# Performance work log

Measured on AMD Instinct MI355X. Metric: run time of the kernel, lower is better.

## Reference

```python
import jax, jax.numpy as jnp
import numpy as np

FREQ_DIM = 64
BLOCK_DIM = 64
N = 256          # lattice sites
CH = 6           # channel_num -> block diagonals at offsets -1, 0, +1
S = 2 * 16 + CH - 2   # seq_num = 36
BS = 4           # block_size (kron of two 2x2 matrices)
HID = 128
EPS = 1e-5
B = 32

_e = np.eye(2)
_sx = np.array([[0., 1.], [1., 0.]])
_siy = np.array([[0., 1.], [-1., 0.]])
_sz = np.array([[1., 0.], [0., -1.]])
_p = [_e, _sx, _siy, _sz]
KRONS = jnp.asarray(np.stack([np.kron(_p[a], _p[b]) for a in range(4) for b in range(4)]).astype(np.float32))  # (16,4,4)
Z1 = KRONS[12]  # kron(sigma_z, I) used for interaction blocks ('z1')


def _bn(h, g, b):
    # BatchNorm1d in training mode: biased batch statistics over axis 0
    mu = h.mean(axis=0)
    v = h.var(axis=0)
    return g * (h - mu) / jnp.sqrt(v + EPS) + b


def _mlp(x, Win, bin_, Wmid, bmid, Wout, bout, gamma, beta):
    # depth-4 MLP: Lin+ReLU, then (BN,Lin,ReLU) x2, then BN,Lin,ReLU
    h = jax.nn.relu(x @ Win + bin_)
    for i in range(Wmid.shape[0]):
        h = jax.nn.relu(_bn(h, gamma[i], beta[i]) @ Wmid[i] + bmid[i])
    return jax.nn.relu(_bn(h, gamma[-1], beta[-1]) @ Wout + bout)


def _lstm(xs, h0, c0, Wih, Whh, bih, bhh):
    # xs: (B, T, S); torch gate order i, f, g, o
    def step(carry, x_t):
        h, c = carry
        gates = x_t @ Wih.T + h @ Whh.T + (bih + bhh)
        i, f, g, o = jnp.split(gates, 4, axis=-1)
        c = jax.nn.sigmoid(f) * c + jax.nn.sigmoid(i) * jnp.tanh(g)
        h = jax.nn.sigmoid(o) * jnp.tanh(c)
        return (h, c), h
    _, hs = jax.lax.scan(step, (h0, c0), jnp.swapaxes(xs, 0, 1))
    return jnp.swapaxes(hs, 0, 1)


def setup_inputs() -> dict:
    key = jax.random.key(0)
    ks = iter(jax.random.split(key, 48))
    def w(shape, s=0.05):
        return jax.random.normal(next(ks), shape, dtype=jnp.float32) * s
    d = {
        'x': w((B, FREQ_DIM + BLOCK_DIM), 1.0),
        'fd_Win': w((FREQ_DIM, HID)), 'fd_bin': w((HID,)),
        'fd_Wmid': w((2, HID, HID)), 'fd_bmid': w((2, HID)),
        'fd_Wout': w((HID, S)), 'fd_bout': w((S,)),
        'fd_gamma': jnp.ones((3, HID), jnp.float32), 'fd_beta': jnp.zeros((3, HID), jnp.float32),
        'bd_Win': w((BLOCK_DIM, HID)), 'bd_bin': w((HID,)),
        'bd_Wmid': w((2, HID, HID)), 'bd_bmid': w((2, HID)),
        'bd_Wout': w((HID, S)), 'bd_bout': w((S,)),
        'bd_gamma': jnp.ones((3, HID), jnp.float32), 'bd_beta': jnp.zeros((3, HID), jnp.float32),
        'sc_Win': w((S, 1, HID)), 'sc_bin': w((S, HID)),
        'sc_Wmid': w((S, 2, HID, HID)), 'sc_bmid': w((S, 2, HID)),
        'sc_Wout': w((S, HID, N)), 'sc_bout': w((S, N)),
        'sc_gamma': jnp.ones((S, 3, HID), jnp.float32), 'sc_beta': jnp.zeros((S, 3, HID), jnp.float32),
        'lstm_Wih': w((4 * S, S)), 'lstm_Whh': w((4 * S, S)),
        'lstm_bih': w((4 * S,)), 'lstm_bhh': w((4 * S,)),
        'mix_W': w((S, 2 * S)), 'mix_b': w((S,)),
    }
    return d


def reference(x, fd_Win, fd_bin, fd_Wmid, fd_bmid, fd_Wout, fd_bout, fd_gamma, fd_beta,
              bd_Win, bd_bin, bd_Wmid, bd_bmid, bd_Wout, bd_bout, bd_gamma, bd_beta,
              sc_Win, sc_bin, sc_Wmid, sc_bmid, sc_Wout, sc_bout, sc_gamma, sc_beta,
              lstm_Wih, lstm_Whh, lstm_bih, lstm_bhh, mix_W, mix_b):
    Bsz = x.shape[0]
    block = _mlp(x[:, FREQ_DIM:], bd_Win, bd_bin, bd_Wmid, bd_bmid, bd_Wout, bd_bout, bd_gamma, bd_beta)  # (B,S)
    freq = _mlp(x[:, :FREQ_DIM], fd_Win, fd_bin, fd_Wmid, fd_bmid, fd_Wout, fd_bout, fd_gamma, fd_beta)   # (B,S)
    # S independent scalar->N MLPs, batched with vmap over the stacked params
    sc = jax.vmap(_mlp)(freq.T[:, :, None], sc_Win, sc_bin, sc_Wmid, sc_bmid,
                        sc_Wout, sc_bout, sc_gamma, sc_beta)  # (S,B,N)
    freq_seq = jnp.cos(sc).transpose(1, 2, 0)   # (B,N,S)
    seq = _lstm(freq_seq, block, jnp.zeros_like(block), lstm_Wih, lstm_Whh, lstm_bih, lstm_bhh)  # (B,N,S)
    block_seq = jnp.concatenate([jnp.broadcast_to(block[:, :, None], (Bsz, S, N)),
                                 jnp.swapaxes(seq, 1, 2)], axis=1)  # (B,2S,N)
    # 1x1 Conv2d == channel mixing matmul
    mixed = jnp.einsum('bcn,oc->bon', block_seq, mix_W) + mix_b[None, :, None]  # (B,S,N)
    inter = mixed[:, :CH - 2]                          # (B,CH-2,N)
    onsite = mixed[:, CH - 2:].reshape(Bsz, 2, 16, N)  # (B,2,16,N)
    H_int = jnp.einsum('bcn,ij->bcnij', inter, Z1)         # (B,CH-2,N,4,4)
    H_os = jnp.einsum('bgkn,kij->bgnij', onsite, KRONS)    # (B,2,N,4,4) summed over 16 pairs
    half = (CH - 2) // 2
    strips = jnp.concatenate([H_int[:, :half], H_os, H_int[:, half:]], axis=1)  # (B,CH,N,4,4)
    strips = strips.reshape(Bsz, CH // 2, 2, N, BS, BS)
    # banded block assembly: strip i lives on block-diagonal offset i - (CH//2)//2
    grid = jnp.zeros((Bsz, 2, N, N, BS, BS), dtype=x.dtype)
    for i in range(CH // 2):
        o = i - (CH // 2) // 2
        rows = jnp.arange(N - abs(o)) + max(0, -o)
        cols = rows + o
        grid = grid.at[:, :, rows, cols].set(strips[:, i][:, :, rows])
    matrix = grid.transpose(0, 1, 2, 4, 3, 5).reshape(Bsz, 2, N * BS, N * BS)
    return matrix
```

## Files before the change

kernel.cpp:

```cpp
#include <hip/hip_runtime.h>
#include <math.h>

#define EPSF 1e-5f

__device__ __forceinline__ float tanhf_fast(float x) {
    return 1.f - 2.f / (__expf(2.f * x) + 1.f);
}

__device__ void mlp64_body(const float* __restrict__ xin,
                           const float* __restrict__ Win,
                           const float* __restrict__ bin_,
                           const float* __restrict__ Wmid,
                           const float* __restrict__ bmid,
                           const float* __restrict__ Wout,
                           const float* __restrict__ bout,
                           const float* __restrict__ gamma,
                           const float* __restrict__ beta,
                           float* __restrict__ out)
{
    __shared__ float sX[32 * 64];
    __shared__ float sA[32 * 128];
    __shared__ float sB[32 * 128];
    __shared__ float sMu[128], sRs[128];
    int tid = threadIdx.x;

    for (int idx = tid; idx < 32 * 64; idx += 256) {
        int b = idx >> 6, c = idx & 63;
        sX[idx] = xin[b * 128 + c];
    }
    __syncthreads();

    for (int idx = tid; idx < 32 * 128; idx += 256) {
        int b = idx >> 7, j = idx & 127;
        float acc = bin_[j];
        for (int c = 0; c < 64; ++c) acc = fmaf(sX[b * 64 + c], Win[c * 128 + j], acc);
        sA[idx] = fmaxf(acc, 0.f);
    }
    __syncthreads();

    float* cur = sA;
    float* nxt = sB;
    for (int l = 0; l < 3; ++l) {
        if (tid < 128) {
            float s = 0.f, s2 = 0.f;
            for (int b = 0; b < 32; ++b) {
                float v = cur[b * 128 + tid];
                s += v; s2 += v * v;
            }
            float mu = s * (1.f / 32.f);
            float var = s2 * (1.f / 32.f) - mu * mu;
            sMu[tid] = mu;
            sRs[tid] = rsqrtf(var + EPSF);
        }
        __syncthreads();
        for (int idx = tid; idx < 32 * 128; idx += 256) {
            int j = idx & 127;
            cur[idx] = gamma[l * 128 + j] * (cur[idx] - sMu[j]) * sRs[j] + beta[l * 128 + j];
        }
        __syncthreads();
        if (l < 2) {
            for (int idx = tid; idx < 32 * 128; idx += 256) {
                int b = idx >> 7, j = idx & 127;
                float acc = bmid[l * 128 + j];
                for (int c = 0; c < 128; ++c)
                    acc = fmaf(cur[b * 128 + c], Wmid[(l * 128 + c) * 128 + j], acc);
                nxt[idx] = fmaxf(acc, 0.f);
            }
            __syncthreads();
            float* t = cur; cur = nxt; nxt = t;
        } else {
            for (int idx = tid; idx < 32 * 36; idx += 256) {
                int b = idx / 36, j = idx - b * 36;
                float acc = bout[j];
                for (int c = 0; c < 128; ++c)
                    acc = fmaf(cur[b * 128 + c], Wout[c * 36 + j], acc);
                out[idx] = fmaxf(acc, 0.f);
            }
        }
    }
}

__global__ __launch_bounds__(256) void k_mlp2(
    const float* __restrict__ x,
    const float* fdWin, const float* fdbin, const float* fdWmid, const float* fdbmid,
    const float* fdWout, const float* fdbout, const float* fdg, const float* fdbt,
    const float* bdWin, const float* bdbin, const float* bdWmid, const float* bdbmid,
    const float* bdWout, const float* bdbout, const float* bdg, const float* bdbt,
    float* freq, float* blk)
{
    if (blockIdx.x == 0)
        mlp64_body(x + 64, bdWin, bdbin, bdWmid, bdbmid, bdWout, bdbout, bdg, bdbt, blk);
    else
        mlp64_body(x, fdWin, fdbin, fdWmid, fdbmid, fdWout, fdbout, fdg, fdbt, freq);
}

__global__ __launch_bounds__(512) void k_sc(
    const float* __restrict__ freq,
    const float* __restrict__ Win,
    const float* __restrict__ bin_,
    const float* __restrict__ Wmid,
    const float* __restrict__ bmid,
    const float* __restrict__ Wout,
    const float* __restrict__ bout,
    const float* __restrict__ gamma,
    const float* __restrict__ beta,
    float* __restrict__ fseq)
{
    int s = blockIdx.x, tid = threadIdx.x;
    __shared__ float sA[32 * 128];
    __shared__ float sB[32 * 128];
    __shared__ float sMu[128], sRs[128];
    const float* Wm = Wmid + (size_t)s * 2 * 128 * 128;
    const float* Wo = Wout + (size_t)s * 128 * 256;
    const float* gm = gamma + s * 3 * 128;
    const float* bt = beta + s * 3 * 128;

    for (int idx = tid; idx < 32 * 128; idx += 512) {
        int b = idx >> 7, j = idx & 127;
        float acc = fmaf(freq[b * 36 + s], Win[s * 128 + j], bin_[s * 128 + j]);
        sA[idx] = fmaxf(acc, 0.f);
    }
    __syncthreads();

    float* cur = sA;
    float* nxt = sB;
    for (int l = 0; l < 3; ++l) {
        if (tid < 128) {
            float sm = 0.f, s2 = 0.f;
            for (int b = 0; b < 32; ++b) {
                float v = cur[b * 128 + tid];
                sm += v; s2 += v * v;
            }
            float mu = sm * (1.f / 32.f);
            float var = s2 * (1.f / 32.f) - mu * mu;
            sMu[tid] = mu;
            sRs[tid] = rsqrtf(var + EPSF);
        }
        __syncthreads();
        for (int idx = tid; idx < 32 * 128; idx += 512) {
            int j = idx & 127;
            cur[idx] = gm[l * 128 + j] * (cur[idx] - sMu[j]) * sRs[j] + bt[l * 128 + j];
        }
        __syncthreads();
        if (l < 2) {
            for (int idx = tid; idx < 32 * 128; idx += 512) {
                int b = idx >> 7, j = idx & 127;
                float acc = bmid[(s * 2 + l) * 128 + j];
                for (int c = 0; c < 128; ++c)
                    acc = fmaf(cur[b * 128 + c], Wm[(l * 128 + c) * 128 + j], acc);
                nxt[idx] = fmaxf(acc, 0.f);
            }
            __syncthreads();
            float* t = cur; cur = nxt; nxt = t;
        } else {
            for (int idx = tid; idx < 32 * 256; idx += 512) {
                int b = idx >> 8, n = idx & 255;
                float acc = bout[s * 256 + n];
                for (int c = 0; c < 128; ++c)
                    acc = fmaf(cur[b * 128 + c], Wo[c * 256 + n], acc);
                float v = fmaxf(acc, 0.f);
                fseq[((size_t)n * 32 + b) * 36 + s] = cosf(v);
            }
        }
    }
}

__global__ __launch_bounds__(512) void k_xg(
    const float* __restrict__ fseq, const float* __restrict__ Wih,
    const float* __restrict__ bih, const float* __restrict__ bhh,
    float* __restrict__ Xg)
{
    int t = blockIdx.x, tid = threadIdx.x;
    __shared__ float sF[32 * 36];
    for (int idx = tid; idx < 1152; idx += 512) sF[idx] = fseq[(size_t)t * 1152 + idx];
    __syncthreads();
    for (int idx = tid; idx < 32 * 144; idx += 512) {
        int b = idx / 144, j = idx - b * 144;
        float acc = bih[j] + bhh[j];
        #pragma unroll
        for (int s2 = 0; s2 < 36; ++s2)
            acc = fmaf(sF[b * 36 + s2], Wih[j * 36 + s2], acc);
        Xg[((size_t)t * 32 + b) * 144 + j] = acc;
    }
}

__global__ __launch_bounds__(192) void k_lstm(
    const float* __restrict__ Xg, const float* __restrict__ blockIn,
    const float* __restrict__ Whh, float* __restrict__ hseq)
{
    int b = blockIdx.x, tid = threadIdx.x;
    __shared__ float sh[36];
    __shared__ float sg[144];
    float w[36];
    if (tid < 144) {
        #pragma unroll
        for (int k = 0; k < 36; ++k) w[k] = Whh[tid * 36 + k];
    }
    if (tid < 36) sh[tid] = blockIn[b * 36 + tid];
    float c = 0.f;
    float xg = (tid < 144) ? Xg[(size_t)b * 144 + tid] : 0.f;
    const int type = tid / 36;
    __syncthreads();

    for (int t = 0; t < 256; ++t) {
        float act = 0.f;
        if (tid < 144) {
            float a0 = 0.f, a1 = 0.f, a2 = 0.f, a3 = 0.f;
            #pragma unroll
            for (int k = 0; k < 36; k += 4) {
                a0 = fmaf(w[k + 0], sh[k + 0], a0);
                a1 = fmaf(w[k + 1], sh[k + 1], a1);
                a2 = fmaf(w[k + 2], sh[k + 2], a2);
                a3 = fmaf(w[k + 3], sh[k + 3], a3);
            }
            float gate = xg + (a0 + a1) + (a2 + a3);
            float sarg = (type == 2) ? 2.f * gate : gate;
            float sv = 1.f / (1.f + __expf(-sarg));
            act = (type == 2) ? 2.f * sv - 1.f : sv;
        }
        if (t < 255 && tid < 144) xg = Xg[((size_t)(t + 1) * 32 + b) * 144 + tid];
        if (tid < 144) sg[tid] = act;
        __syncthreads();
        if (tid < 36) {
            float iv = sg[tid], fv = sg[36 + tid], gv = sg[72 + tid], ov = sg[108 + tid];
            c = fmaf(fv, c, iv * gv);
            float h = ov * tanhf_fast(c);
            sh[tid] = h;
            hseq[((size_t)b * 256 + t) * 36 + tid] = h;
        }
        __syncthreads();
    }
}

__global__ __launch_bounds__(256) void k_mixed(
    const float* __restrict__ blockIn, const float* __restrict__ hseq,
    const float* __restrict__ mixW, const float* __restrict__ mixb,
    float* __restrict__ mixed)
{
    int wg = blockIdx.x;
    int b = wg / 36, o = wg - b * 36;
    int n = threadIdx.x;
    float acc = mixb[o];
    const float* wrow = mixW + o * 72;
    const float* blk = blockIn + b * 36;
    #pragma unroll
    for (int c = 0; c < 36; ++c) acc = fmaf(wrow[c], blk[c], acc);
    const float* hp = hseq + ((size_t)b * 256 + n) * 36;
    #pragma unroll
    for (int u = 0; u < 36; ++u) acc = fmaf(wrow[36 + u], hp[u], acc);
    mixed[(size_t)wg * 256 + n] = acc;
}

__device__ __forceinline__ float pauliv(int p, int r, int c) {
    switch (p) {
        case 0: return (r == c) ? 1.f : 0.f;
        case 1: return (r != c) ? 1.f : 0.f;
        case 2: return (r == 0 && c == 1) ? 1.f : ((r == 1 && c == 0) ? -1.f : 0.f);
        default: return (r == c) ? ((r == 0) ? 1.f : -1.f) : 0.f;
    }
}

__global__ __launch_bounds__(256) void k_asm(
    const float* __restrict__ mixed, float* __restrict__ out)
{
    int wg = blockIdx.x;
    int n = wg & 255, bg = wg >> 8;
    int g = bg & 1, b = bg >> 1;
    int tid = threadIdx.x;
    __shared__ float sD[16];
    __shared__ float sEdge[2];
    if (tid < 16) {
        int r = tid >> 2, c = tid & 3;
        float acc = 0.f;
        #pragma unroll
        for (int k = 0; k < 16; ++k) {
            float kv = pauliv(k >> 2, r >> 1, c >> 1) * pauliv(k & 3, r & 1, c & 1);
            acc = fmaf(mixed[((size_t)b * 36 + 4 + 16 * g + k) * 256 + n], kv, acc);
        }
        sD[tid] = acc;
    } else if (tid == 16) {
        sEdge[0] = mixed[((size_t)b * 36 + g) * 256 + n];
    } else if (tid == 17) {
        sEdge[1] = mixed[((size_t)b * 36 + 2 + g) * 256 + n];
    }
    __syncthreads();

    float4* outp = (float4*)out + ((size_t)bg * 1024 + 4 * n) * 256;
    int m = tid;
    if (m == n) {
        #pragma unroll
        for (int r = 0; r < 4; ++r)
            outp[r * 256 + m] = make_float4(sD[r * 4 + 0], sD[r * 4 + 1], sD[r * 4 + 2], sD[r * 4 + 3]);
    } else if (m == n - 1) {
        float v = sEdge[0];
        outp[0 * 256 + m] = make_float4(v, 0.f, 0.f, 0.f);
        outp[1 * 256 + m] = make_float4(0.f, v, 0.f, 0.f);
        outp[2 * 256 + m] = make_float4(0.f, 0.f, -v, 0.f);
        outp[3 * 256 + m] = make_float4(0.f, 0.f, 0.f, -v);
    } else if (m == n + 1) {
        float v = sEdge[1];
        outp[0 * 256 + m] = make_float4(v, 0.f, 0.f, 0.f);
        outp[1 * 256 + m] = make_float4(0.f, v, 0.f, 0.f);
        outp[2 * 256 + m] = make_float4(0.f, 0.f, -v, 0.f);
        outp[3 * 256 + m] = make_float4(0.f, 0.f, 0.f, -v);
    } else {
        float4 z = make_float4(0.f, 0.f, 0.f, 0.f);
        #pragma unroll
        for (int r = 0; r < 4; ++r) outp[r * 256 + m] = z;
    }
}

extern "C" void kernel_launch(void* const* d_in, const int* in_sizes, int n_in,
                              void* d_out, int out_size, void* d_ws, size_t ws_size,
                              hipStream_t stream) {
    const float* x      = (const float*)d_in[0];
    const float* fdWin  = (const float*)d_in[1];
    const float* fdbin  = (const float*)d_in[2];
    const float* fdWmid = (const float*)d_in[3];
    const float* fdbmid = (const float*)d_in[4];
    const float* fdWout = (const float*)d_in[5];
    const float* fdbout = (const float*)d_in[6];
    const float* fdg    = (const float*)d_in[7];
    const float* fdbt   = (const float*)d_in[8];
    const float* bdWin  = (const float*)d_in[9];
    const float* bdbin  = (const float*)d_in[10];
    const float* bdWmid = (const float*)d_in[11];
    const float* bdbmid = (const float*)d_in[12];
    const float* bdWout = (const float*)d_in[13];
    const float* bdbout = (const float*)d_in[14];
    const float* bdg    = (const float*)d_in[15];
    const float* bdbt   = (const float*)d_in[16];
    const float* scWin  = (const float*)d_in[17];
    const float* scbin  = (const float*)d_in[18];
    const float* scWmid = (const float*)d_in[19];
    const float* scbmid = (const float*)d_in[20];
    const float* scWout = (const float*)d_in[21];
    const float* scbout = (const float*)d_in[22];
    const float* scg    = (const float*)d_in[23];
    const float* scbt   = (const float*)d_in[24];
    const float* Wih    = (const float*)d_in[25];
    const float* Whh    = (const float*)d_in[26];
    const float* bih    = (const float*)d_in[27];
    const float* bhh    = (const float*)d_in[28];
    const float* mixW   = (const float*)d_in[29];
    const float* mixb   = (const float*)d_in[30];

    float* ws    = (float*)d_ws;
    float* freq  = ws;
    float* blk   = ws + 1152;
    float* fseq  = ws + 2304;
    float* Xg    = ws + 297216;
    float* hseq  = ws + 1476864;
    float* mixed = ws + 1771776;

    k_mlp2<<<2, 256, 0, stream>>>(x,
        fdWin, fdbin, fdWmid, fdbmid, fdWout, fdbout, fdg, fdbt,
        bdWin, bdbin, bdWmid, bdbmid, bdWout, bdbout, bdg, bdbt,
        freq, blk);
    k_sc<<<36, 512, 0, stream>>>(freq, scWin, scbin, scWmid, scbmid,
                                 scWout, scbout, scg, scbt, fseq);
    k_xg<<<256, 512, 0, stream>>>(fseq, Wih, bih, bhh, Xg);
    k_lstm<<<32, 192, 0, stream>>>(Xg, blk, Whh, hseq);
    k_mixed<<<1152, 256, 0, stream>>>(blk, hseq, mixW, mixb, mixed);
    k_asm<<<16384, 256, 0, stream>>>(mixed, (float*)d_out);
}
```

Measured before the change: 375.6 us.

## Fuse all stages into one cooperative persistent kernel with grid syncs

Replaces the six separate launches (MLPs, per-sequence MLPs, input-gate projection, LSTM, channel mixing, banded assembly) with a single cooperative kernel of 256 blocks of 512 threads, using grid.sync between stages. It also overlaps the block MLP with the sequence MLPs, stages a transposed Wih in shared memory, and switches cosf to __cosf. The goal is to remove launch overhead and inter-kernel gaps. The cost is that the 16M-element output assembly now runs on only 256 blocks looping 32 times, and grid syncs leave most blocks idle during the serial LSTM.

```diff
diff --git a/kernel.cpp b/kernel.cpp
--- a/kernel.cpp
+++ b/kernel.cpp
@@ -1,10 +1,30 @@
 #include <hip/hip_runtime.h>
+#include <hip/hip_cooperative_groups.h>
 #include <math.h>
 
+namespace cg = cooperative_groups;
+
 #define EPSF 1e-5f
 
-__device__ __forceinline__ float tanhf_fast(float x) {
-    return 1.f - 2.f / (__expf(2.f * x) + 1.f);
+struct Params {
+    const float *x;
+    const float *fdWin, *fdbin, *fdWmid, *fdbmid, *fdWout, *fdbout, *fdg, *fdbt;
+    const float *bdWin, *bdbin, *bdWmid, *bdbmid, *bdWout, *bdbout, *bdg, *bdbt;
+    const float *scWin, *scbin, *scWmid, *scbmid, *scWout, *scbout, *scg, *scbt;
+    const float *Wih, *Whh, *bih, *bhh, *mixW, *mixb;
+    float *freq, *blk, *fseq, *Xg, *hseq, *mixed, *out;
+};
+
+__device__ __forceinline__ float sigmf(float x) { return 1.f / (1.f + __expf(-x)); }
+__device__ __forceinline__ float tanhf_fast(float x) { return 1.f - 2.f / (__expf(2.f * x) + 1.f); }
+
+__device__ __forceinline__ float pauliv(int p, int r, int c) {
+    switch (p) {
+        case 0: return (r == c) ? 1.f : 0.f;
+        case 1: return (r != c) ? 1.f : 0.f;
+        case 2: return (r == 0 && c == 1) ? 1.f : ((r == 1 && c == 0) ? -1.f : 0.f);
+        default: return (r == c) ? ((r == 0) ? 1.f : -1.f) : 0.f;
+    }
 }
 
 __device__ void mlp64_body(const float* __restrict__ xin,
@@ -16,21 +36,23 @@
                            const float* __restrict__ bout,
                            const float* __restrict__ gamma,
                            const float* __restrict__ beta,
-                           float* __restrict__ out)
+                           float* __restrict__ out,
+                           float* sm)
 {
-    __shared__ float sX[32 * 64];
-    __shared__ float sA[32 * 128];
-    __shared__ float sB[32 * 128];
-    __shared__ float sMu[128], sRs[128];
+    float* sX  = sm;
+    float* sA  = sm + 2048;
+    float* sB  = sm + 6144;
+    float* sMu = sm + 10240;
+    float* sRs = sm + 10368;
     int tid = threadIdx.x;
 
-    for (int idx = tid; idx < 32 * 64; idx += 256) {
+    for (int idx = tid; idx < 2048; idx += 512) {
         int b = idx >> 6, c = idx & 63;
         sX[idx] = xin[b * 128 + c];
     }
     __syncthreads();
 
-    for (int idx = tid; idx < 32 * 128; idx += 256) {
+    for (int idx = tid; idx < 4096; idx += 512) {
         int b = idx >> 7, j = idx & 127;
         float acc = bin_[j];
         for (int c = 0; c < 64; ++c) acc = fmaf(sX[b * 64 + c], Win[c * 128 + j], acc);
@@ -53,13 +75,13 @@
             sRs[tid] = rsqrtf(var + EPSF);
         }
         __syncthreads();
-        for (int idx = tid; idx < 32 * 128; idx += 256) {
+        for (int idx = tid; idx < 4096; idx += 512) {
             int j = idx & 127;
             cur[idx] = gamma[l * 128 + j] * (cur[idx] - sMu[j]) * sRs[j] + beta[l * 128 + j];
         }
         __syncthreads();
         if (l < 2) {
-            for (int idx = tid; idx < 32 * 128; idx += 256) {
+            for (int idx = tid; idx < 4096; idx += 512) {
                 int b = idx >> 7, j = idx & 127;
                 float acc = bmid[l * 128 + j];
                 for (int c = 0; c < 128; ++c)
@@ -69,7 +91,7 @@
             __syncthreads();
             float* t = cur; cur = nxt; nxt = t;
         } else {
-            for (int idx = tid; idx < 32 * 36; idx += 256) {
+            for (int idx = tid; idx < 32 * 36; idx += 512) {
                 int b = idx / 36, j = idx - b * 36;
                 float acc = bout[j];
                 for (int c = 0; c < 128; ++c)
@@ -80,44 +102,21 @@
     }
 }
 
-__global__ __launch_bounds__(256) void k_mlp2(
-    const float* __restrict__ x,
-    const float* fdWin, const float* fdbin, const float* fdWmid, const float* fdbmid,
-    const float* fdWout, const float* fdbout, const float* fdg, const float* fdbt,
-    const float* bdWin, const float* bdbin, const float* bdWmid, const float* bdbmid,
-    const float* bdWout, const float* bdbout, const float* bdg, const float* bdbt,
-    float* freq, float* blk)
+__device__ void sc_body(int s, const Params& p, float* sm)
 {
-    if (blockIdx.x == 0)
-        mlp64_body(x + 64, bdWin, bdbin, bdWmid, bdbmid, bdWout, bdbout, bdg, bdbt, blk);
-    else
-        mlp64_body(x, fdWin, fdbin, fdWmid, fdbmid, fdWout, fdbout, fdg, fdbt, freq);
-}
-
-__global__ __launch_bounds__(512) void k_sc(
-    const float* __restrict__ freq,
-    const float* __restrict__ Win,
-    const float* __restrict__ bin_,
-    const float* __restrict__ Wmid,
-    const float* __restrict__ bmid,
-    const float* __restrict__ Wout,
-    const float* __restrict__ bout,
-    const float* __restrict__ gamma,
-    const float* __restrict__ beta,
-    float* __restrict__ fseq)
-{
-    int s = blockIdx.x, tid = threadIdx.x;
-    __shared__ float sA[32 * 128];
-    __shared__ float sB[32 * 128];
-    __shared__ float sMu[128], sRs[128];
-    const float* Wm = Wmid + (size_t)s * 2 * 128 * 128;
-    const float* Wo = Wout + (size_t)s * 128 * 256;
-    const float* gm = gamma + s * 3 * 128;
-    const float* bt = beta + s * 3 * 128;
-
-    for (int idx = tid; idx < 32 * 128; idx += 512) {
+    float* sA  = sm;
+    float* sB  = sm + 4096;
+    float* sMu = sm + 8192;
+    float* sRs = sm + 8320;
+    int tid = threadIdx.x;
+    const float* Wm = p.scWmid + (size_t)s * 2 * 128 * 128;
+    const float* Wo = p.scWout + (size_t)s * 128 * 256;
+    const float* gm = p.scg + s * 3 * 128;
+    const float* bt = p.scbt + s * 3 * 128;
+
+    for (int idx = tid; idx < 4096; idx += 512) {
         int b = idx >> 7, j = idx & 127;
-        float acc = fmaf(freq[b * 36 + s], Win[s * 128 + j], bin_[s * 128 + j]);
+        float acc = fmaf(p.freq[b * 36 + s], p.scWin[s * 128 + j], p.scbin[s * 128 + j]);
         sA[idx] = fmaxf(acc, 0.f);
     }
     __syncthreads();
@@ -126,26 +125,26 @@
     float* nxt = sB;
     for (int l = 0; l < 3; ++l) {
         if (tid < 128) {
-            float sm = 0.f, s2 = 0.f;
+            float sm_ = 0.f, s2 = 0.f;
             for (int b = 0; b < 32; ++b) {
                 float v = cur[b * 128 + tid];
-                sm += v; s2 += v * v;
-            }
-            float mu = sm * (1.f / 32.f);
+                sm_ += v; s2 += v * v;
+            }
+            float mu = sm_ * (1.f / 32.f);
             float var = s2 * (1.f / 32.f) - mu * mu;
             sMu[tid] = mu;
             sRs[tid] = rsqrtf(var + EPSF);
         }
         __syncthreads();
-        for (int idx = tid; idx < 32 * 128; idx += 512) {
+        for (int idx = tid; idx < 4096; idx += 512) {
             int j = idx & 127;
             cur[idx] = gm[l * 128 + j] * (cur[idx] - sMu[j]) * sRs[j] + bt[l * 128 + j];
         }
         __syncthreads();
         if (l < 2) {
-            for (int idx = tid; idx < 32 * 128; idx += 512) {
+            for (int idx = tid; idx < 4096; idx += 512) {
                 int b = idx >> 7, j = idx & 127;
-                float acc = bmid[(s * 2 + l) * 128 + j];
+                float acc = p.scbmid[(s * 2 + l) * 128 + j];
                 for (int c = 0; c < 128; ++c)
                     acc = fmaf(cur[b * 128 + c], Wm[(l * 128 + c) * 128 + j], acc);
                 nxt[idx] = fmaxf(acc, 0.f);
@@ -155,212 +154,221 @@
         } else {
             for (int idx = tid; idx < 32 * 256; idx += 512) {
                 int b = idx >> 8, n = idx & 255;
-                float acc = bout[s * 256 + n];
+                float acc = p.scbout[s * 256 + n];
                 for (int c = 0; c < 128; ++c)
                     acc = fmaf(cur[b * 128 + c], Wo[c * 256 + n], acc);
                 float v = fmaxf(acc, 0.f);
-                fseq[((size_t)n * 32 + b) * 36 + s] = cosf(v);
-            }
-        }
-    }
-}
-
-__global__ __launch_bounds__(512) void k_xg(
-    const float* __restrict__ fseq, const float* __restrict__ Wih,
-    const float* __restrict__ bih, const float* __restrict__ bhh,
-    float* __restrict__ Xg)
+                p.fseq[((size_t)n * 32 + b) * 36 + s] = __cosf(v);
+            }
+        }
+    }
+}
+
+__global__ __launch_bounds__(512, 1) void fused_hamgen(Params p)
 {
-    int t = blockIdx.x, tid = threadIdx.x;
-    __shared__ float sF[32 * 36];
-    for (int idx = tid; idx < 1152; idx += 512) sF[idx] = fseq[(size_t)t * 1152 + idx];
-    __syncthreads();
-    for (int idx = tid; idx < 32 * 144; idx += 512) {
-        int b = idx / 144, j = idx - b * 144;
-        float acc = bih[j] + bhh[j];
-        #pragma unroll
-        for (int s2 = 0; s2 < 36; ++s2)
-            acc = fmaf(sF[b * 36 + s2], Wih[j * 36 + s2], acc);
-        Xg[((size_t)t * 32 + b) * 144 + j] = acc;
-    }
-}
-
-__global__ __launch_bounds__(192) void k_lstm(
-    const float* __restrict__ Xg, const float* __restrict__ blockIn,
-    const float* __restrict__ Whh, float* __restrict__ hseq)
-{
-    int b = blockIdx.x, tid = threadIdx.x;
-    __shared__ float sh[36];
-    __shared__ float sg[144];
-    float w[36];
-    if (tid < 144) {
-        #pragma unroll
-        for (int k = 0; k < 36; ++k) w[k] = Whh[tid * 36 + k];
-    }
-    if (tid < 36) sh[tid] = blockIn[b * 36 + tid];
-    float c = 0.f;
-    float xg = (tid < 144) ? Xg[(size_t)b * 144 + tid] : 0.f;
-    const int type = tid / 36;
-    __syncthreads();
-
-    for (int t = 0; t < 256; ++t) {
-        float act = 0.f;
+    cg::grid_group grid = cg::this_grid();
+    __shared__ float sm[10496];
+    const int bid = blockIdx.x;
+    const int tid = threadIdx.x;
+
+    if (bid == 0)
+        mlp64_body(p.x, p.fdWin, p.fdbin, p.fdWmid, p.fdbmid, p.fdWout, p.fdbout,
+                   p.fdg, p.fdbt, p.freq, sm);
+    grid.sync();
+
+    if (bid < 36) {
+        sc_body(bid, p, sm);
+    } else if (bid == 36) {
+        mlp64_body(p.x + 64, p.bdWin, p.bdbin, p.bdWmid, p.bdbmid, p.bdWout, p.bdbout,
+                   p.bdg, p.bdbt, p.blk, sm);
+    }
+    grid.sync();
+
+    {
+        int t = bid;
+        float* sF  = sm;
+        float* sWt = sm + 1152;
+        for (int idx = tid; idx < 1152; idx += 512) sF[idx] = p.fseq[(size_t)t * 1152 + idx];
+        for (int idx = tid; idx < 5184; idx += 512) {
+            int j = idx / 36, s2 = idx - j * 36;
+            sWt[s2 * 144 + j] = p.Wih[idx];
+        }
+        __syncthreads();
+        for (int idx = tid; idx < 4608; idx += 512) {
+            int b = idx / 144, j = idx - b * 144;
+            float acc = p.bih[j] + p.bhh[j];
+            #pragma unroll
+            for (int s2 = 0; s2 < 36; ++s2)
+                acc = fmaf(sF[b * 36 + s2], sWt[s2 * 144 + j], acc);
+            p.Xg[(size_t)t * 4608 + idx] = acc;
+        }
+    }
+    grid.sync();
+
+    if (bid < 32) {
+        int b = bid;
+        float* sh = sm;
+        float* sg = sm + 64;
+        float w[36];
         if (tid < 144) {
-            float a0 = 0.f, a1 = 0.f, a2 = 0.f, a3 = 0.f;
             #pragma unroll
-            for (int k = 0; k < 36; k += 4) {
-                a0 = fmaf(w[k + 0], sh[k + 0], a0);
-                a1 = fmaf(w[k + 1], sh[k + 1], a1);
-                a2 = fmaf(w[k + 2], sh[k + 2], a2);
-                a3 = fmaf(w[k + 3], sh[k + 3], a3);
-            }
-            float gate = xg + (a0 + a1) + (a2 + a3);
-            float sarg = (type == 2) ? 2.f * gate : gate;
-            float sv = 1.f / (1.f + __expf(-sarg));
-            act = (type == 2) ? 2.f * sv - 1.f : sv;
-        }
-        if (t < 255 && tid < 144) xg = Xg[((size_t)(t + 1) * 32 + b) * 144 + tid];
-        if (tid < 144) sg[tid] = act;
-        __syncthreads();
-        if (tid < 36) {
-            float iv = sg[tid], fv = sg[36 + tid], gv = sg[72 + tid], ov = sg[108 + tid];
-            c = fmaf(fv, c, iv * gv);
-            float h = ov * tanhf_fast(c);
-            sh[tid] = h;
-            hseq[((size_t)b * 256 + t) * 36 + tid] = h;
-        }
-        __syncthreads();
-    }
-}
-
-__global__ __launch_bounds__(256) void k_mixed(
-    const float* __restrict__ blockIn, const float* __restrict__ hseq,
-    const float* __restrict__ mixW, const float* __restrict__ mixb,
-    float* __restrict__ mixed)
-{
-    int wg = blockIdx.x;
-    int b = wg / 36, o = wg - b * 36;
-    int n = threadIdx.x;
-    float acc = mixb[o];
-    const float* wrow = mixW + o * 72;
-    const float* blk = blockIn + b * 36;
-    #pragma unroll
-    for (int c = 0; c < 36; ++c) acc = fmaf(wrow[c], blk[c], acc);
-    const float* hp = hseq + ((size_t)b * 256 + n) * 36;
-    #pragma unroll
-    for (int u = 0; u < 36; ++u) acc = fmaf(wrow[36 + u], hp[u], acc);
-    mixed[(size_t)wg * 256 + n] = acc;
-}
-
-__device__ __forceinline__ float pauliv(int p, int r, int c) {
-    switch (p) {
-        case 0: return (r == c) ? 1.f : 0.f;
-        case 1: return (r != c) ? 1.f : 0.f;
-        case 2: return (r == 0 && c == 1) ? 1.f : ((r == 1 && c == 0) ? -1.f : 0.f);
-        default: return (r == c) ? ((r == 0) ? 1.f : -1.f) : 0.f;
-    }
-}
-
-__global__ __launch_bounds__(256) void k_asm(
-    const float* __restrict__ mixed, float* __restrict__ out)
-{
-    int wg = blockIdx.x;
-    int n = wg & 255, bg = wg >> 8;
-    int g = bg & 1, b = bg >> 1;
-    int tid = threadIdx.x;
-    __shared__ float sD[16];
-    __shared__ float sEdge[2];
-    if (tid < 16) {
-        int r = tid >> 2, c = tid & 3;
-        float acc = 0.f;
-        #pragma unroll
-        for (int k = 0; k < 16; ++k) {
-            float kv = pauliv(k >> 2, r >> 1, c >> 1) * pauliv(k & 3, r & 1, c & 1);
-            acc = fmaf(mixed[((size_t)b * 36 + 4 + 16 * g + k) * 256 + n], kv, acc);
-        }
-        sD[tid] = acc;
-    } else if (tid == 16) {
-        sEdge[0] = mixed[((size_t)b * 36 + g) * 256 + n];
-    } else if (tid == 17) {
-        sEdge[1] = mixed[((size_t)b * 36 + 2 + g) * 256 + n];
-    }
-    __syncthreads();
-
-    float4* outp = (float4*)out + ((size_t)bg * 1024 + 4 * n) * 256;
-    int m = tid;
-    if (m == n) {
-        #pragma unroll
-        for (int r = 0; r < 4; ++r)
-            outp[r * 256 + m] = make_float4(sD[r * 4 + 0], sD[r * 4 + 1], sD[r * 4 + 2], sD[r * 4 + 3]);
-    } else if (m == n - 1) {
-        float v = sEdge[0];
-        outp[0 * 256 + m] = make_float4(v, 0.f, 0.f, 0.f);
-        outp[1 * 256 + m] = make_float4(0.f, v, 0.f, 0.f);
-        outp[2 * 256 + m] = make_float4(0.f, 0.f, -v, 0.f);
-        outp[3 * 256 + m] = make_float4(0.f, 0.f, 0.f, -v);
-    } else if (m == n + 1) {
-        float v = sEdge[1];
-        outp[0 * 256 + m] = make_float4(v, 0.f, 0.f, 0.f);
-        outp[1 * 256 + m] = make_float4(0.f, v, 0.f, 0.f);
-        outp[2 * 256 + m] = make_float4(0.f, 0.f, -v, 0.f);
-        outp[3 * 256 + m] = make_float4(0.f, 0.f, 0.f, -v);
-    } else {
-        float4 z = make_float4(0.f, 0.f, 0.f, 0.f);
-        #pragma unroll
-        for (int r = 0; r < 4; ++r) outp[r * 256 + m] = z;
+            for (int k = 0; k < 36; ++k) w[k] = p.Whh[tid * 36 + k];
+        }
+        if (tid < 36) sh[tid] = p.blk[b * 36 + tid];
+        float c = 0.f;
+        float xg = (tid < 144) ? p.Xg[(size_t)b * 144 + tid] : 0.f;
+        const int type = tid / 36;
+        __syncthreads();
+
+        for (int t = 0; t < 256; ++t) {
+            float act = 0.f;
+            if (tid < 144) {
+                float a0 = 0.f, a1 = 0.f, a2 = 0.f, a3 = 0.f;
+                #pragma unroll
+                for (int k = 0; k < 36; k += 4) {
+                    a0 = fmaf(w[k + 0], sh[k + 0], a0);
+                    a1 = fmaf(w[k + 1], sh[k + 1], a1);
+                    a2 = fmaf(w[k + 2], sh[k + 2], a2);
+                    a3 = fmaf(w[k + 3], sh[k + 3], a3);
+                }
+                float gate = xg + (a0 + a1) + (a2 + a3);
+                float sarg = (type == 2) ? 2.f * gate : gate;
+                float sv = sigmf(sarg);
+                act = (type == 2) ? 2.f * sv - 1.f : sv;
+            }
+            if (t < 255 && tid < 144) xg = p.Xg[((size_t)(t + 1) * 32 + b) * 144 + tid];
+            if (tid < 144) sg[tid] = act;
+            __syncthreads();
+            if (tid < 36) {
+                float iv = sg[tid], fv = sg[36 + tid], gv = sg[72 + tid], ov = sg[108 + tid];
+                c = fmaf(fv, c, iv * gv);
+                float h = ov * tanhf_fast(c);
+                sh[tid] = h;
+                p.hseq[((size_t)b * 256 + t) * 36 + tid] = h;
+            }
+            __syncthreads();
+        }
+    }
+    grid.sync();
+
+    {
+        int n = tid & 255;
+        int half = tid >> 8;
+        for (int job = bid * 2 + half; job < 1152; job += 512) {
+            int b = job / 36, o = job - (job / 36) * 36;
+            float acc = p.mixb[o];
+            const float* wrow = p.mixW + o * 72;
+            const float* bl = p.blk + b * 36;
+            #pragma unroll
+            for (int c2 = 0; c2 < 36; ++c2) acc = fmaf(wrow[c2], bl[c2], acc);
+            const float* hp = p.hseq + ((size_t)b * 256 + n) * 36;
+            #pragma unroll
+            for (int u = 0; u < 36; ++u) acc = fmaf(wrow[36 + u], hp[u], acc);
+            p.mixed[(size_t)job * 256 + n] = acc;
+        }
+    }
+    grid.sync();
+
+    {
+        float* sChan = sm;
+        float* sD    = sm + 40;
+        int n = bid;
+        int half = tid >> 8;
+        int m = tid & 255;
+        for (int iter = 0; iter < 32; ++iter) {
+            int bg = iter * 2 + half;
+            int g = bg & 1, b = bg >> 1;
+            if (m < 18) {
+                int ch = (m == 0) ? g : ((m == 1) ? 2 + g : 4 + 16 * g + (m - 2));
+                sChan[half * 18 + m] = p.mixed[((size_t)(b * 36 + ch)) * 256 + n];
+            }
+            __syncthreads();
+            if (m < 16) {
+                int r = m >> 2, cc = m & 3;
+                float acc = 0.f;
+                #pragma unroll
+                for (int k = 0; k < 16; ++k) {
+                    float kv = pauliv(k >> 2, r >> 1, cc >> 1) * pauliv(k & 3, r & 1, cc & 1);
+                    acc = fmaf(sChan[half * 18 + 2 + k], kv, acc);
+                }
+                sD[half * 16 + m] = acc;
+            }
+            __syncthreads();
+
+            float4* outp = (float4*)p.out + ((size_t)bg * 1024 + 4 * n) * 256;
+            const float* d = sD + half * 16;
+            if (m == n) {
+                #pragma unroll
+                for (int r = 0; r < 4; ++r)
+                    outp[r * 256 + m] = make_float4(d[r * 4 + 0], d[r * 4 + 1], d[r * 4 + 2], d[r * 4 + 3]);
+            } else if (m == n - 1) {
+                float v = sChan[half * 18 + 0];
+                outp[0 * 256 + m] = make_float4(v, 0.f, 0.f, 0.f);
+                outp[1 * 256 + m] = make_float4(0.f, v, 0.f, 0.f);
+                outp[2 * 256 + m] = make_float4(0.f, 0.f, -v, 0.f);
+                outp[3 * 256 + m] = make_float4(0.f, 0.f, 0.f, -v);
+            } else if (m == n + 1) {
+                float v = sChan[half * 18 + 1];
+                outp[0 * 256 + m] = make_float4(v, 0.f, 0.f, 0.f);
+                outp[1 * 256 + m] = make_float4(0.f, v, 0.f, 0.f);
+                outp[2 * 256 + m] = make_float4(0.f, 0.f, -v, 0.f);
+                outp[3 * 256 + m] = make_float4(0.f, 0.f, 0.f, -v);
+            } else {
+                float4 z = make_float4(0.f, 0.f, 0.f, 0.f);
+                #pragma unroll
+                for (int r = 0; r < 4; ++r) outp[r * 256 + m] = z;
+            }
+            __syncthreads();
+        }
     }
 }
 
 extern "C" void kernel_launch(void* const* d_in, const int* in_sizes, int n_in,
                               void* d_out, int out_size, void* d_ws, size_t ws_size,
                               hipStream_t stream) {
-    const float* x      = (const float*)d_in[0];
-    const float* fdWin  = (const float*)d_in[1];
-    const float* fdbin  = (const float*)d_in[2];
-    const float* fdWmid = (const float*)d_in[3];
-    const float* fdbmid = (const float*)d_in[4];
-    const float* fdWout = (const float*)d_in[5];
-    const float* fdbout = (const float*)d_in[6];
-    const float* fdg    = (const float*)d_in[7];
-    const float* fdbt   = (const float*)d_in[8];
-    const float* bdWin  = (const float*)d_in[9];
-    const float* bdbin  = (const float*)d_in[10];
-    const float* bdWmid = (const float*)d_in[11];
-    const float* bdbmid = (const float*)d_in[12];
-    const float* bdWout = (const float*)d_in[13];
-    const float* bdbout = (const float*)d_in[14];
-    const float* bdg    = (const float*)d_in[15];
-    const float* bdbt   = (const float*)d_in[16];
-    const float* scWin  = (const float*)d_in[17];
-    const float* scbin  = (const float*)d_in[18];
-    const float* scWmid = (const float*)d_in[19];
-    const float* scbmid = (const float*)d_in[20];
-    const float* scWout = (const float*)d_in[21];
-    const float* scbout = (const float*)d_in[22];
-    const float* scg    = (const float*)d_in[23];
-    const float* scbt   = (const float*)d_in[24];
-    const float* Wih    = (const float*)d_in[25];
-    const float* Whh    = (const float*)d_in[26];
-    const float* bih    = (const float*)d_in[27];
-    const float* bhh    = (const float*)d_in[28];
-    const float* mixW   = (const float*)d_in[29];
-    const float* mixb   = (const float*)d_in[30];
-
-    float* ws    = (float*)d_ws;
-    float* freq  = ws;
-    float* blk   = ws + 1152;
-    float* fseq  = ws + 2304;
-    float* Xg    = ws + 297216;
-    float* hseq  = ws + 1476864;
-    float* mixed = ws + 1771776;
-
-    k_mlp2<<<2, 256, 0, stream>>>(x,
-        fdWin, fdbin, fdWmid, fdbmid, fdWout, fdbout, fdg, fdbt,
-        bdWin, bdbin, bdWmid, bdbmid, bdWout, bdbout, bdg, bdbt,
-        freq, blk);
-    k_sc<<<36, 512, 0, stream>>>(freq, scWin, scbin, scWmid, scbmid,
-                                 scWout, scbout, scg, scbt, fseq);
-    k_xg<<<256, 512, 0, stream>>>(fseq, Wih, bih, bhh, Xg);
-    k_lstm<<<32, 192, 0, stream>>>(Xg, blk, Whh, hseq);
-    k_mixed<<<1152, 256, 0, stream>>>(blk, hseq, mixW, mixb, mixed);
-    k_asm<<<16384, 256, 0, stream>>>(mixed, (float*)d_out);
-}
+    Params p;
+    p.x      = (const float*)d_in[0];
+    p.fdWin  = (const float*)d_in[1];
+    p.fdbin  = (const float*)d_in[2];
+    p.fdWmid = (const float*)d_in[3];
+    p.fdbmid = (const float*)d_in[4];
+    p.fdWout = (const float*)d_in[5];
+    p.fdbout = (const float*)d_in[6];
+    p.fdg    = (const float*)d_in[7];
+    p.fdbt   = (const float*)d_in[8];
+    p.bdWin  = (const float*)d_in[9];
+    p.bdbin  = (const float*)d_in[10];
+    p.bdWmid = (const float*)d_in[11];
+    p.bdbmid = (const float*)d_in[12];
+    p.bdWout = (const float*)d_in[13];
+    p.bdbout = (const float*)d_in[14];
+    p.bdg    = (const float*)d_in[15];
+    p.bdbt   = (const float*)d_in[16];
+    p.scWin  = (const float*)d_in[17];
+    p.scbin  = (const float*)d_in[18];
+    p.scWmid = (const float*)d_in[19];
+    p.scbmid = (const float*)d_in[20];
+    p.scWout = (const float*)d_in[21];
+    p.scbout = (const float*)d_in[22];
+    p.scg    = (const float*)d_in[23];
+    p.scbt   = (const float*)d_in[24];
+    p.Wih    = (const float*)d_in[25];
+    p.Whh    = (const float*)d_in[26];
+    p.bih    = (const float*)d_in[27];
+    p.bhh    = (const float*)d_in[28];
+    p.mixW   = (const float*)d_in[29];
+    p.mixb   = (const float*)d_in[30];
+
+    float* ws = (float*)d_ws;
+    p.freq  = ws;
+    p.blk   = ws + 1152;
+    p.fseq  = ws + 2304;
+    p.Xg    = ws + 297216;
+    p.hseq  = ws + 1476864;
+    p.mixed = ws + 1771776;
+    p.out   = (float*)d_out;
+
+    void* args[] = { (void*)&p };
+    hipLaunchCooperativeKernel((void*)fused_hamgen, dim3(256), dim3(512),
+                               args, 0, stream);
+}
```

After: 453.4 us. 20.7% more time.
